# Kernel tuning notes

Measured on AMD Instinct MI355X. Metric: run time of the kernel, lower is better.

Reference implementation:

```python
import jax, jax.numpy as jnp
import numpy as np

N_NODES = 50000
N_EDGES = 800000
IN_CH = 128
OUT_CH = 64
HEADS = 4
NEG_SLOPE = 0.2


def gat_layer(x, src, dst, W, a_src, a_dst, b, n):
    """One GATConv (PyG semantics, self-loops already in src/dst).
    x:[n,Fin], W:[Fin,H*C], a_src/a_dst:[H,C], b:[H*C]. Returns [n,H*C] (concat heads)."""
    H, C = a_src.shape
    h = (x @ W).reshape(n, H, C)                      # [n,H,C]
    alpha_s = jnp.einsum('nhc,hc->nh', h, a_src)      # [n,H]
    alpha_d = jnp.einsum('nhc,hc->nh', h, a_dst)
    e = jax.nn.leaky_relu(alpha_s[src] + alpha_d[dst], NEG_SLOPE)  # [E,H]
    m = jax.ops.segment_max(e, dst, num_segments=n)   # per-dst-node max (stable softmax)
    p = jnp.exp(e - m[dst])
    denom = jax.ops.segment_sum(p, dst, num_segments=n)
    alpha = p / (denom[dst] + 1e-16)                  # [E,H]
    out = jax.ops.segment_sum(h[src] * alpha[:, :, None], dst, num_segments=n)
    return out.reshape(n, H * C) + b


def setup_inputs() -> dict:
    key = jax.random.key(0)
    ks = jax.random.split(key, 10)
    x = jax.random.normal(ks[0], (N_NODES, IN_CH), dtype=jnp.float32)
    edge_index = jax.random.randint(ks[1], (2, N_EDGES), 0, N_NODES, dtype=jnp.int64)
    s = 0.05
    W1 = jax.random.normal(ks[2], (IN_CH, HEADS * OUT_CH), dtype=jnp.float32) * s
    a_src1 = jax.random.normal(ks[3], (HEADS, OUT_CH), dtype=jnp.float32) * s
    a_dst1 = jax.random.normal(ks[4], (HEADS, OUT_CH), dtype=jnp.float32) * s
    b1 = jnp.zeros((HEADS * OUT_CH,), dtype=jnp.float32)
    W2 = jax.random.normal(ks[5], (HEADS * OUT_CH, OUT_CH), dtype=jnp.float32) * s
    a_src2 = jax.random.normal(ks[6], (1, OUT_CH), dtype=jnp.float32) * s
    a_dst2 = jax.random.normal(ks[7], (1, OUT_CH), dtype=jnp.float32) * s
    b2 = jnp.zeros((OUT_CH,), dtype=jnp.float32)
    return {"x": x, "edge_index": edge_index, "W1": W1, "a_src1": a_src1,
            "a_dst1": a_dst1, "b1": b1, "W2": W2, "a_src2": a_src2,
            "a_dst2": a_dst2, "b2": b2}


def reference(x, edge_index, W1, a_src1, a_dst1, b1, W2, a_src2, a_dst2, b2):
    n = x.shape[0]
    # PyG GATConv adds self-loops by default
    loops = jnp.arange(n, dtype=edge_index.dtype)
    src = jnp.concatenate([edge_index[0], loops])
    dst = jnp.concatenate([edge_index[1], loops])
    h = jax.nn.relu(gat_layer(x, src, dst, W1, a_src1, a_dst1, b1, n))
    return gat_layer(h, src, dst, W2, a_src2, a_dst2, b2, n)
```

## Files before the change

kernel.cpp:

```cpp
#include <hip/hip_runtime.h>
#include <math.h>

#define N_NODES   50000
#define E0_EDGES  800000
#define E_TOT     (E0_EDGES + N_NODES)
#define FIN       128
#define F1        256
#define H1        4
#define C2        64
#define NEG_SLOPE 0.2f

typedef short bf16x8 __attribute__((ext_vector_type(8)));
typedef float f32x4  __attribute__((ext_vector_type(4)));

__device__ __forceinline__ unsigned short f2bf(float f) {
  unsigned u = __float_as_uint(f);
  u = (u + 0x7FFFu + ((u >> 16) & 1u)) >> 16;
  return (unsigned short)u;
}
__device__ __forceinline__ float bf2f(unsigned short h) {
  return __uint_as_float((unsigned)h << 16);
}
__device__ __forceinline__ float leaky(float v) {
  return v >= 0.f ? v : NEG_SLOPE * v;
}

__global__ __launch_bounds__(256) void deg_kernel(
    const int* __restrict__ ei, int* __restrict__ count) {
  int e = blockIdx.x * 256 + threadIdx.x;
  if (e >= E_TOT) return;
  int dst = (e < E0_EDGES) ? ei[E0_EDGES + e] : (e - E0_EDGES);
  atomicAdd(&count[dst], 1);
}

__global__ __launch_bounds__(256) void scanA_kernel(
    const int* __restrict__ cnt, int* __restrict__ bsum, int n) {
  int i = blockIdx.x * 256 + threadIdx.x;
  int v = (i < n) ? cnt[i] : 0;
#pragma unroll
  for (int d = 1; d < 64; d <<= 1) v += __shfl_xor(v, d);
  __shared__ int ws[4];
  if ((threadIdx.x & 63) == 0) ws[threadIdx.x >> 6] = v;
  __syncthreads();
  if (threadIdx.x == 0) bsum[blockIdx.x] = ws[0] + ws[1] + ws[2] + ws[3];
}

__global__ __launch_bounds__(256) void scanB_kernel(
    const int* __restrict__ bsum, int* __restrict__ bexcl,
    int* __restrict__ off_n, int nb) {
  const int t = threadIdx.x, lane = t & 63, wid = t >> 6;
  int v = (t < nb) ? bsum[t] : 0;
  int sv = v;
#pragma unroll
  for (int d = 1; d < 64; d <<= 1) {
    int u = __shfl_up(sv, d);
    if (lane >= d) sv += u;
  }
  __shared__ int ws[4];
  if (lane == 63) ws[wid] = sv;
  __syncthreads();
  int add = 0;
  for (int k = 0; k < wid; ++k) add += ws[k];
  int incl = sv + add;
  if (t < nb) bexcl[t] = incl - v;
  if (t == 255) off_n[0] = incl;
}

__global__ __launch_bounds__(256) void scanC_kernel(
    const int* __restrict__ cnt, const int* __restrict__ bexcl,
    int* __restrict__ off, int n) {
  const int t = threadIdx.x, lane = t & 63, wid = t >> 6;
  int i = blockIdx.x * 256 + t;
  int v = (i < n) ? cnt[i] : 0;
  int sv = v;
#pragma unroll
  for (int d = 1; d < 64; d <<= 1) {
    int u = __shfl_up(sv, d);
    if (lane >= d) sv += u;
  }
  __shared__ int ws[4];
  if (lane == 63) ws[wid] = sv;
  __syncthreads();
  int add = 0;
  for (int k = 0; k < wid; ++k) add += ws[k];
  if (i < n) off[i] = sv + add - v + bexcl[blockIdx.x];
}

__global__ __launch_bounds__(256) void scatter_w_kernel(
    const int* __restrict__ ei, const int* __restrict__ offset,
    int* __restrict__ cursor, int* __restrict__ csr_src,
    const float* __restrict__ as1, const float* __restrict__ ad1,
    float* __restrict__ w4) {
  int e = blockIdx.x * 256 + threadIdx.x;
  if (e >= E_TOT) return;
  int src, dst;
  if (e < E0_EDGES) { src = ei[e]; dst = ei[E0_EDGES + e]; }
  else              { src = e - E0_EDGES; dst = src; }
  int pos = offset[dst] + atomicAdd(&cursor[dst], 1);
  csr_src[pos] = src;
  const float4 s4 = *reinterpret_cast<const float4*>(&as1[src * H1]);
  const float4 d4 = *reinterpret_cast<const float4*>(&ad1[dst * H1]);
  float4 w;
  w.x = __expf(leaky(s4.x + d4.x));
  w.y = __expf(leaky(s4.y + d4.y));
  w.z = __expf(leaky(s4.z + d4.z));
  w.w = __expf(leaky(s4.w + d4.w));
  *reinterpret_cast<float4*>(&w4[(size_t)pos * 4]) = w;
}

__global__ __launch_bounds__(256) void gemm1_kernel(
    const float* __restrict__ A, const float* __restrict__ B,
    unsigned short* __restrict__ C, float* __restrict__ as1,
    float* __restrict__ ad1, const float* __restrict__ a_s,
    const float* __restrict__ a_d, int M) {
  constexpr int K = FIN, BN = 128, KP = K + 8, NF = BN / 16;
  __shared__ unsigned short BT[BN * KP];
  const int tid = threadIdx.x, lane = tid & 63, wid = tid >> 6;
  const int gy = blockIdx.y, n0 = gy * BN;

  for (int idx = tid; idx < K * (BN / 8); idx += 256) {
    int k = idx >> 4;
    int c = idx & 15;
    const float* src = &B[(size_t)k * F1 + n0 + c * 8];
    float4 lo = *reinterpret_cast<const float4*>(src);
    float4 hi = *reinterpret_cast<const float4*>(src + 4);
    int nb = c * 8;
    BT[(nb + 0) * KP + k] = f2bf(lo.x); BT[(nb + 1) * KP + k] = f2bf(lo.y);
    BT[(nb + 2) * KP + k] = f2bf(lo.z); BT[(nb + 3) * KP + k] = f2bf(lo.w);
    BT[(nb + 4) * KP + k] = f2bf(hi.x); BT[(nb + 5) * KP + k] = f2bf(hi.y);
    BT[(nb + 6) * KP + k] = f2bf(hi.z); BT[(nb + 7) * KP + k] = f2bf(hi.w);
  }
  __syncthreads();

  const int r0 = (blockIdx.x * 4 + wid) * 16;
  if (r0 >= M) return;
  const int nlane = lane & 15;
  const int kg    = (lane >> 4) * 8;
  const int arow  = min(r0 + nlane, M - 1);

  f32x4 acc[NF];
#pragma unroll
  for (int nf = 0; nf < NF; ++nf) acc[nf] = (f32x4){0.f, 0.f, 0.f, 0.f};

  const float* ap = &A[(size_t)arow * K + kg];
#pragma unroll
  for (int kk = 0; kk < K; kk += 32) {
    float4 v0 = *reinterpret_cast<const float4*>(ap + kk);
    float4 v1 = *reinterpret_cast<const float4*>(ap + kk + 4);
    bf16x8 a;
    a[0] = (short)f2bf(v0.x); a[1] = (short)f2bf(v0.y);
    a[2] = (short)f2bf(v0.z); a[3] = (short)f2bf(v0.w);
    a[4] = (short)f2bf(v1.x); a[5] = (short)f2bf(v1.y);
    a[6] = (short)f2bf(v1.z); a[7] = (short)f2bf(v1.w);
#pragma unroll
    for (int nf = 0; nf < NF; ++nf) {
      bf16x8 b = *reinterpret_cast<const bf16x8*>(&BT[(nf * 16 + nlane) * KP + kk + kg]);
      acc[nf] = __builtin_amdgcn_mfma_f32_16x16x32_bf16(a, b, acc[nf], 0, 0, 0);
    }
  }

  const int crow = r0 + (lane >> 4) * 4;
#pragma unroll
  for (int nf = 0; nf < NF; ++nf) {
    const int cc = n0 + nf * 16 + nlane;
#pragma unroll
    for (int j = 0; j < 4; ++j) {
      int rr = crow + j;
      if (rr < M) C[(size_t)rr * F1 + cc] = f2bf(acc[nf][j]);
    }
  }

#pragma unroll
  for (int j = 0; j < 4; ++j) {
    float ps0 = 0.f, ps1 = 0.f, pd0 = 0.f, pd1 = 0.f;
#pragma unroll
    for (int nf = 0; nf < NF; ++nf) {
      int col = n0 + nf * 16 + nlane;
      float v = acc[nf][j];
      float sc = a_s[col], dc = a_d[col];
      if (nf < 4) { ps0 = fmaf(v, sc, ps0); pd0 = fmaf(v, dc, pd0); }
      else        { ps1 = fmaf(v, sc, ps1); pd1 = fmaf(v, dc, pd1); }
    }
#pragma unroll
    for (int d = 1; d < 16; d <<= 1) {
      ps0 += __shfl_xor(ps0, d); ps1 += __shfl_xor(ps1, d);
      pd0 += __shfl_xor(pd0, d); pd1 += __shfl_xor(pd1, d);
    }
    int row = crow + j;
    if (nlane == 0 && row < M) {
      float2 s2 = {ps0, ps1}, d2 = {pd0, pd1};
      *reinterpret_cast<float2*>(&as1[row * 4 + gy * 2]) = s2;
      *reinterpret_cast<float2*>(&ad1[row * 4 + gy * 2]) = d2;
    }
  }
}

__global__ __launch_bounds__(256) void gemm2_kernel(
    const unsigned short* __restrict__ A, const float* __restrict__ B,
    unsigned short* __restrict__ C, float* __restrict__ as2,
    float* __restrict__ ad2, const float* __restrict__ a_s,
    const float* __restrict__ a_d, int M) {
  constexpr int K = F1, BN = 64, KP = K + 8, NF = BN / 16;
  __shared__ unsigned short BT[BN * KP];
  const int tid = threadIdx.x, lane = tid & 63, wid = tid >> 6;

  for (int idx = tid; idx < K * (BN / 8); idx += 256) {
    int k = idx >> 3;
    int c = idx & 7;
    const float* src = &B[(size_t)k * C2 + c * 8];
    float4 lo = *reinterpret_cast<const float4*>(src);
    float4 hi = *reinterpret_cast<const float4*>(src + 4);
    int nb = c * 8;
    BT[(nb + 0) * KP + k] = f2bf(lo.x); BT[(nb + 1) * KP + k] = f2bf(lo.y);
    BT[(nb + 2) * KP + k] = f2bf(lo.z); BT[(nb + 3) * KP + k] = f2bf(lo.w);
    BT[(nb + 4) * KP + k] = f2bf(hi.x); BT[(nb + 5) * KP + k] = f2bf(hi.y);
    BT[(nb + 6) * KP + k] = f2bf(hi.z); BT[(nb + 7) * KP + k] = f2bf(hi.w);
  }
  __syncthreads();

  const int r0 = (blockIdx.x * 4 + wid) * 16;
  if (r0 >= M) return;
  const int nlane = lane & 15;
  const int kg    = (lane >> 4) * 8;
  const int arow  = min(r0 + nlane, M - 1);

  f32x4 acc[NF];
#pragma unroll
  for (int nf = 0; nf < NF; ++nf) acc[nf] = (f32x4){0.f, 0.f, 0.f, 0.f};

  const unsigned short* ap = &A[(size_t)arow * K + kg];
#pragma unroll
  for (int kk = 0; kk < K; kk += 32) {
    bf16x8 a = *reinterpret_cast<const bf16x8*>(ap + kk);
#pragma unroll
    for (int nf = 0; nf < NF; ++nf) {
      bf16x8 b = *reinterpret_cast<const bf16x8*>(&BT[(nf * 16 + nlane) * KP + kk + kg]);
      acc[nf] = __builtin_amdgcn_mfma_f32_16x16x32_bf16(a, b, acc[nf], 0, 0, 0);
    }
  }

  const int crow = r0 + (lane >> 4) * 4;
#pragma unroll
  for (int nf = 0; nf < NF; ++nf) {
    const int cc = nf * 16 + nlane;
#pragma unroll
    for (int j = 0; j < 4; ++j) {
      int rr = crow + j;
      if (rr < M) C[(size_t)rr * C2 + cc] = f2bf(acc[nf][j]);
    }
  }

#pragma unroll
  for (int j = 0; j < 4; ++j) {
    float ps = 0.f, pd = 0.f;
#pragma unroll
    for (int nf = 0; nf < NF; ++nf) {
      int col = nf * 16 + nlane;
      float v = acc[nf][j];
      ps = fmaf(v, a_s[col], ps);
      pd = fmaf(v, a_d[col], pd);
    }
#pragma unroll
    for (int d = 1; d < 16; d <<= 1) {
      ps += __shfl_xor(ps, d);
      pd += __shfl_xor(pd, d);
    }
    int row = crow + j;
    if (nlane == 0 && row < M) { as2[row] = ps; ad2[row] = pd; }
  }
}

__global__ __launch_bounds__(256) void aggregate1_kernel(
    const unsigned short* __restrict__ h1b, const float* __restrict__ w4,
    const int* __restrict__ csr_src, const int* __restrict__ offset,
    const float* __restrict__ b1, unsigned short* __restrict__ out1b,
    int node0, int n) {
  const int lane = threadIdx.x & 63;
  const int node = node0 + blockIdx.x * 4 + (threadIdx.x >> 6);
  if (node >= n) return;
  const int beg = offset[node], end = offset[node + 1];
  const int hl = lane >> 4;
  const unsigned loff = (unsigned)(lane * 4);

  float4 acc = make_float4(0.f, 0.f, 0.f, 0.f);
  float den = 0.f;
  int e = beg;
  for (; e + 7 < end; e += 8) {
    int s[8];
    float wv[8];
    ushort4 r[8];
#pragma unroll
    for (int i = 0; i < 8; ++i) s[i] = csr_src[e + i];
#pragma unroll
    for (int i = 0; i < 8; ++i) wv[i] = w4[(size_t)(e + i) * 4 + hl];
#pragma unroll
    for (int i = 0; i < 8; ++i)
      r[i] = *reinterpret_cast<const ushort4*>(h1b + (unsigned)(s[i] * F1) + loff);
#pragma unroll
    for (int i = 0; i < 8; ++i) {
      den += wv[i];
      acc.x = fmaf(wv[i], bf2f(r[i].x), acc.x);
      acc.y = fmaf(wv[i], bf2f(r[i].y), acc.y);
      acc.z = fmaf(wv[i], bf2f(r[i].z), acc.z);
      acc.w = fmaf(wv[i], bf2f(r[i].w), acc.w);
    }
  }
  for (; e < end; ++e) {
    const int s0 = csr_src[e];
    const float w = w4[(size_t)e * 4 + hl];
    den += w;
    const ushort4 r0 = *reinterpret_cast<const ushort4*>(h1b + (unsigned)(s0 * F1) + loff);
    acc.x = fmaf(w, bf2f(r0.x), acc.x);
    acc.y = fmaf(w, bf2f(r0.y), acc.y);
    acc.z = fmaf(w, bf2f(r0.z), acc.z);
    acc.w = fmaf(w, bf2f(r0.w), acc.w);
  }
  const float inv = 1.f / (den + 1e-16f);
  const float4 bb = *reinterpret_cast<const float4*>(&b1[lane * 4]);
  ushort4 ob;
  ob.x = f2bf(fmaxf(fmaf(acc.x, inv, bb.x), 0.f));
  ob.y = f2bf(fmaxf(fmaf(acc.y, inv, bb.y), 0.f));
  ob.z = f2bf(fmaxf(fmaf(acc.z, inv, bb.z), 0.f));
  ob.w = f2bf(fmaxf(fmaf(acc.w, inv, bb.w), 0.f));
  *reinterpret_cast<ushort4*>(&out1b[(size_t)node * F1 + lane * 4]) = ob;
}

__global__ __launch_bounds__(256) void aggregate2_kernel(
    const unsigned short* __restrict__ h2b, const float* __restrict__ as,
    const float* __restrict__ ad, const int* __restrict__ csr_src,
    const int* __restrict__ offset, const float* __restrict__ b2,
    float* __restrict__ out, int n) {
  const int lane = threadIdx.x & 63;
  const int node = blockIdx.x * 4 + (threadIdx.x >> 6);
  if (node >= n) return;
  const int beg = offset[node], end = offset[node + 1];
  const float adv = ad[node];

  float acc = 0.f;
  float den = 0.f;
  int e = beg;
  for (; e + 7 < end; e += 8) {
    int s[8];
    unsigned short r[8];
    float a[8];
#pragma unroll
    for (int i = 0; i < 8; ++i) s[i] = csr_src[e + i];
#pragma unroll
    for (int i = 0; i < 8; ++i) r[i] = h2b[(unsigned)(s[i] * C2) + lane];
#pragma unroll
    for (int i = 0; i < 8; ++i) a[i] = as[s[i]];
#pragma unroll
    for (int i = 0; i < 8; ++i) {
      const float w = __expf(leaky(a[i] + adv));
      den += w;
      acc = fmaf(w, bf2f(r[i]), acc);
    }
  }
  for (; e < end; ++e) {
    const int s0 = csr_src[e];
    const float w = __expf(leaky(as[s0] + adv));
    den += w;
    acc = fmaf(w, bf2f(h2b[(unsigned)(s0 * C2) + lane]), acc);
  }
  out[(size_t)node * C2 + lane] = fmaf(acc, 1.f / (den + 1e-16f), b2[lane]);
}

extern "C" void kernel_launch(void* const* d_in, const int* in_sizes, int n_in,
                              void* d_out, int out_size, void* d_ws, size_t ws_size,
                              hipStream_t stream) {
  const float* x      = (const float*)d_in[0];
  const int*   ei     = (const int*)d_in[1];
  const float* W1     = (const float*)d_in[2];
  const float* a_src1 = (const float*)d_in[3];
  const float* a_dst1 = (const float*)d_in[4];
  const float* b1     = (const float*)d_in[5];
  const float* W2     = (const float*)d_in[6];
  const float* a_src2 = (const float*)d_in[7];
  const float* a_dst2 = (const float*)d_in[8];
  const float* b2     = (const float*)d_in[9];
  float*       out    = (float*)d_out;

  const int n = N_NODES;
  const int nchunks = (n + 255) / 256;

  char* w = (char*)d_ws;
  unsigned short* h1b   = (unsigned short*)w; w += (size_t)n * F1 * 2;
  unsigned short* out1b = (unsigned short*)w; w += (size_t)n * F1 * 2;
  float*          w4    = (float*)w;          w += (size_t)E_TOT * 4 * 4;
  float*          as1   = (float*)w;          w += (size_t)n * H1 * 4;
  float*          ad1   = (float*)w;          w += (size_t)n * H1 * 4;
  float*          as2   = (float*)w;          w += 200192;
  float*          ad2   = (float*)w;          w += 200192;
  int*            cnt   = (int*)w;            w += 200192;
  int*            cur   = (int*)w;            w += 200192;
  int*            off   = (int*)w;            w += 200704;
  int*            bsum  = (int*)w;            w += 1024;
  int*            bexcl = (int*)w;            w += 1024;
  int*            csr   = (int*)w;            w += 3400192;
  unsigned short* h2b   = h1b;

  hipMemsetAsync(cnt, 0, 2 * 200192, stream);
  deg_kernel<<<(E_TOT + 255) / 256, 256, 0, stream>>>(ei, cnt);
  scanA_kernel<<<nchunks, 256, 0, stream>>>(cnt, bsum, n);
  scanB_kernel<<<1, 256, 0, stream>>>(bsum, bexcl, &off[n], nchunks);
  scanC_kernel<<<nchunks, 256, 0, stream>>>(cnt, bexcl, off, n);

  {
    dim3 grid((n + 63) / 64, 2);
    gemm1_kernel<<<grid, 256, 0, stream>>>(x, W1, h1b, as1, ad1, a_src1, a_dst1, n);
  }

  scatter_w_kernel<<<(E_TOT + 255) / 256, 256, 0, stream>>>(
      ei, off, cur, csr, as1, ad1, w4);

  {
    const int half = 25000;
    aggregate1_kernel<<<(half + 3) / 4, 256, 0, stream>>>(
        h1b, w4, csr, off, b1, out1b, 0, half);
    aggregate1_kernel<<<(n - half + 3) / 4, 256, 0, stream>>>(
        h1b, w4, csr, off, b1, out1b, half, n);
  }

  {
    dim3 grid((n + 63) / 64, 1);
    gemm2_kernel<<<grid, 256, 0, stream>>>(out1b, W2, h2b, as2, ad2, a_src2, a_dst2, n);
  }
  aggregate2_kernel<<<(n + 3) / 4, 256, 0, stream>>>(h2b, as2, ad2, csr, off, b2, out, n);
}
```

Measured before the change: 333.6 us.

## Split edge-weight computation into CSR-ordered kernels for both layers

The scatter kernel now only builds the CSR source array, and the layer-1 attention weights move to a separate per-node kernel that walks CSR order. Writes to w4 become contiguous instead of scattered by atomic position, and scatter can run before gemm1. Layer 2 gets a similar precompute kernel for its edge weights, so aggregate2 reads w2 sequentially instead of gathering as2 and computing exp inline. This adds two launches and an extra pass over csr_src.

```diff
diff --git a/kernel.cpp b/kernel.cpp
--- a/kernel.cpp
+++ b/kernel.cpp
@@ -86,11 +86,9 @@
   if (i < n) off[i] = sv + add - v + bexcl[blockIdx.x];
 }
 
-__global__ __launch_bounds__(256) void scatter_w_kernel(
+__global__ __launch_bounds__(256) void scatter_kernel(
     const int* __restrict__ ei, const int* __restrict__ offset,
-    int* __restrict__ cursor, int* __restrict__ csr_src,
-    const float* __restrict__ as1, const float* __restrict__ ad1,
-    float* __restrict__ w4) {
+    int* __restrict__ cursor, int* __restrict__ csr_src) {
   int e = blockIdx.x * 256 + threadIdx.x;
   if (e >= E_TOT) return;
   int src, dst;
@@ -98,14 +96,40 @@
   else              { src = e - E0_EDGES; dst = src; }
   int pos = offset[dst] + atomicAdd(&cursor[dst], 1);
   csr_src[pos] = src;
-  const float4 s4 = *reinterpret_cast<const float4*>(&as1[src * H1]);
-  const float4 d4 = *reinterpret_cast<const float4*>(&ad1[dst * H1]);
-  float4 w;
-  w.x = __expf(leaky(s4.x + d4.x));
-  w.y = __expf(leaky(s4.y + d4.y));
-  w.z = __expf(leaky(s4.z + d4.z));
-  w.w = __expf(leaky(s4.w + d4.w));
-  *reinterpret_cast<float4*>(&w4[(size_t)pos * 4]) = w;
+}
+
+__global__ __launch_bounds__(256) void w1_kernel(
+    const float* __restrict__ as1, const float* __restrict__ ad1,
+    const int* __restrict__ csr_src, const int* __restrict__ offset,
+    float* __restrict__ w4, int n) {
+  const int lane = threadIdx.x & 63;
+  const int node = blockIdx.x * 4 + (threadIdx.x >> 6);
+  if (node >= n) return;
+  const int beg = offset[node], end = offset[node + 1];
+  const float4 d4 = *reinterpret_cast<const float4*>(&ad1[node * H1]);
+  for (int e = beg + lane; e < end; e += 64) {
+    const int s = csr_src[e];
+    const float4 s4 = *reinterpret_cast<const float4*>(&as1[s * H1]);
+    float4 w;
+    w.x = __expf(leaky(s4.x + d4.x));
+    w.y = __expf(leaky(s4.y + d4.y));
+    w.z = __expf(leaky(s4.z + d4.z));
+    w.w = __expf(leaky(s4.w + d4.w));
+    *reinterpret_cast<float4*>(&w4[(size_t)e * 4]) = w;
+  }
+}
+
+__global__ __launch_bounds__(256) void w2_kernel(
+    const float* __restrict__ as2, const float* __restrict__ ad2,
+    const int* __restrict__ csr_src, const int* __restrict__ offset,
+    float* __restrict__ w2, int n) {
+  const int lane = threadIdx.x & 63;
+  const int node = blockIdx.x * 4 + (threadIdx.x >> 6);
+  if (node >= n) return;
+  const int beg = offset[node], end = offset[node + 1];
+  const float dv = ad2[node];
+  for (int e = beg + lane; e < end; e += 64)
+    w2[e] = __expf(leaky(as2[csr_src[e]] + dv));
 }
 
 __global__ __launch_bounds__(256) void gemm1_kernel(
@@ -326,39 +350,36 @@
 }
 
 __global__ __launch_bounds__(256) void aggregate2_kernel(
-    const unsigned short* __restrict__ h2b, const float* __restrict__ as,
-    const float* __restrict__ ad, const int* __restrict__ csr_src,
-    const int* __restrict__ offset, const float* __restrict__ b2,
-    float* __restrict__ out, int n) {
+    const unsigned short* __restrict__ h2b, const float* __restrict__ w2,
+    const int* __restrict__ csr_src, const int* __restrict__ offset,
+    const float* __restrict__ b2, float* __restrict__ out, int n) {
   const int lane = threadIdx.x & 63;
   const int node = blockIdx.x * 4 + (threadIdx.x >> 6);
   if (node >= n) return;
   const int beg = offset[node], end = offset[node + 1];
-  const float adv = ad[node];
 
   float acc = 0.f;
   float den = 0.f;
   int e = beg;
   for (; e + 7 < end; e += 8) {
     int s[8];
+    float wv[8];
     unsigned short r[8];
-    float a[8];
 #pragma unroll
     for (int i = 0; i < 8; ++i) s[i] = csr_src[e + i];
 #pragma unroll
+    for (int i = 0; i < 8; ++i) wv[i] = w2[e + i];
+#pragma unroll
     for (int i = 0; i < 8; ++i) r[i] = h2b[(unsigned)(s[i] * C2) + lane];
 #pragma unroll
-    for (int i = 0; i < 8; ++i) a[i] = as[s[i]];
-#pragma unroll
     for (int i = 0; i < 8; ++i) {
-      const float w = __expf(leaky(a[i] + adv));
-      den += w;
-      acc = fmaf(w, bf2f(r[i]), acc);
+      den += wv[i];
+      acc = fmaf(wv[i], bf2f(r[i]), acc);
     }
   }
   for (; e < end; ++e) {
     const int s0 = csr_src[e];
-    const float w = __expf(leaky(as[s0] + adv));
+    const float w = w2[e];
     den += w;
     acc = fmaf(w, bf2f(h2b[(unsigned)(s0 * C2) + lane]), acc);
   }
@@ -398,21 +419,20 @@
   int*            bexcl = (int*)w;            w += 1024;
   int*            csr   = (int*)w;            w += 3400192;
   unsigned short* h2b   = h1b;
+  float*          w2    = w4;
 
   hipMemsetAsync(cnt, 0, 2 * 200192, stream);
   deg_kernel<<<(E_TOT + 255) / 256, 256, 0, stream>>>(ei, cnt);
   scanA_kernel<<<nchunks, 256, 0, stream>>>(cnt, bsum, n);
   scanB_kernel<<<1, 256, 0, stream>>>(bsum, bexcl, &off[n], nchunks);
   scanC_kernel<<<nchunks, 256, 0, stream>>>(cnt, bexcl, off, n);
+  scatter_kernel<<<(E_TOT + 255) / 256, 256, 0, stream>>>(ei, off, cur, csr);
 
   {
     dim3 grid((n + 63) / 64, 2);
     gemm1_kernel<<<grid, 256, 0, stream>>>(x, W1, h1b, as1, ad1, a_src1, a_dst1, n);
   }
-
-  scatter_w_kernel<<<(E_TOT + 255) / 256, 256, 0, stream>>>(
-      ei, off, cur, csr, as1, ad1, w4);
-
+  w1_kernel<<<(n + 3) / 4, 256, 0, stream>>>(as1, ad1, csr, off, w4, n);
   {
     const int half = 25000;
     aggregate1_kernel<<<(half + 3) / 4, 256, 0, stream>>>(
@@ -425,5 +445,6 @@
     dim3 grid((n + 63) / 64, 1);
     gemm2_kernel<<<grid, 256, 0, stream>>>(out1b, W2, h2b, as2, ad2, a_src2, a_dst2, n);
   }
-  aggregate2_kernel<<<(n + 3) / 4, 256, 0, stream>>>(h2b, as2, ad2, csr, off, b2, out, n);
-}
+  w2_kernel<<<(n + 3) / 4, 256, 0, stream>>>(as2, ad2, csr, off, w2, n);
+  aggregate2_kernel<<<(n + 3) / 4, 256, 0, stream>>>(h2b, w2, csr, off, b2, out, n);
+}
```

Result: slower. 354.0 us (+6.1%).

## Record edge ranks in degree pass and fuse CSR scatter into GEMM1 launch

Applied to the files above, without the earlier changes.

The degree-count kernel now stores each edge's atomic rank, so the CSR scatter needs no second atomic cursor. That scatter runs as extra blocks inside the GEMM1 launch so the two overlap. Edge weights are computed in a separate node-centric kernel over CSR order, which reads the destination score once per node, and aggregate1 runs as a single launch instead of two halves. In exchange there is an extra rank buffer write and read, and one more pass over the CSR edges.

```diff
diff --git a/kernel.cpp b/kernel.cpp
--- a/kernel.cpp
+++ b/kernel.cpp
@@ -10,6 +10,10 @@
 #define C2        64
 #define NEG_SLOPE 0.2f
 
+#define NBX1      ((N_NODES + 63) / 64)
+#define GEMM1_BLOCKS (NBX1 * 2)
+#define SCAT_BLOCKS  ((E_TOT + 255) / 256)
+
 typedef short bf16x8 __attribute__((ext_vector_type(8)));
 typedef float f32x4  __attribute__((ext_vector_type(4)));
 
@@ -26,11 +30,12 @@
 }
 
 __global__ __launch_bounds__(256) void deg_kernel(
-    const int* __restrict__ ei, int* __restrict__ count) {
+    const int* __restrict__ ei, int* __restrict__ count,
+    int* __restrict__ rank) {
   int e = blockIdx.x * 256 + threadIdx.x;
   if (e >= E_TOT) return;
   int dst = (e < E0_EDGES) ? ei[E0_EDGES + e] : (e - E0_EDGES);
-  atomicAdd(&count[dst], 1);
+  rank[e] = atomicAdd(&count[dst], 1);
 }
 
 __global__ __launch_bounds__(256) void scanA_kernel(
@@ -86,37 +91,31 @@
   if (i < n) off[i] = sv + add - v + bexcl[blockIdx.x];
 }
 
-__global__ __launch_bounds__(256) void scatter_w_kernel(
-    const int* __restrict__ ei, const int* __restrict__ offset,
-    int* __restrict__ cursor, int* __restrict__ csr_src,
-    const float* __restrict__ as1, const float* __restrict__ ad1,
-    float* __restrict__ w4) {
-  int e = blockIdx.x * 256 + threadIdx.x;
-  if (e >= E_TOT) return;
-  int src, dst;
-  if (e < E0_EDGES) { src = ei[e]; dst = ei[E0_EDGES + e]; }
-  else              { src = e - E0_EDGES; dst = src; }
-  int pos = offset[dst] + atomicAdd(&cursor[dst], 1);
-  csr_src[pos] = src;
-  const float4 s4 = *reinterpret_cast<const float4*>(&as1[src * H1]);
-  const float4 d4 = *reinterpret_cast<const float4*>(&ad1[dst * H1]);
-  float4 w;
-  w.x = __expf(leaky(s4.x + d4.x));
-  w.y = __expf(leaky(s4.y + d4.y));
-  w.z = __expf(leaky(s4.z + d4.z));
-  w.w = __expf(leaky(s4.w + d4.w));
-  *reinterpret_cast<float4*>(&w4[(size_t)pos * 4]) = w;
-}
-
-__global__ __launch_bounds__(256) void gemm1_kernel(
+__global__ __launch_bounds__(256) void gemm1_scatter_kernel(
     const float* __restrict__ A, const float* __restrict__ B,
     unsigned short* __restrict__ C, float* __restrict__ as1,
     float* __restrict__ ad1, const float* __restrict__ a_s,
-    const float* __restrict__ a_d, int M) {
+    const float* __restrict__ a_d, int M,
+    const int* __restrict__ ei, const int* __restrict__ offset,
+    const int* __restrict__ rank, int* __restrict__ csr_src) {
   constexpr int K = FIN, BN = 128, KP = K + 8, NF = BN / 16;
   __shared__ unsigned short BT[BN * KP];
+  const int bid = blockIdx.x;
+
+  if (bid >= GEMM1_BLOCKS) {
+    int e = (bid - GEMM1_BLOCKS) * 256 + threadIdx.x;
+    if (e >= E_TOT) return;
+    int src, dst;
+    if (e < E0_EDGES) { src = ei[e]; dst = ei[E0_EDGES + e]; }
+    else              { src = e - E0_EDGES; dst = src; }
+    csr_src[offset[dst] + rank[e]] = src;
+    return;
+  }
+
+  const int bx = bid % NBX1;
+  const int gy = bid / NBX1;
   const int tid = threadIdx.x, lane = tid & 63, wid = tid >> 6;
-  const int gy = blockIdx.y, n0 = gy * BN;
+  const int n0 = gy * BN;
 
   for (int idx = tid; idx < K * (BN / 8); idx += 256) {
     int k = idx >> 4;
@@ -132,7 +131,7 @@
   }
   __syncthreads();
 
-  const int r0 = (blockIdx.x * 4 + wid) * 16;
+  const int r0 = (bx * 4 + wid) * 16;
   if (r0 >= M) return;
   const int nlane = lane & 15;
   const int kg    = (lane >> 4) * 8;
@@ -192,6 +191,27 @@
       *reinterpret_cast<float2*>(&as1[row * 4 + gy * 2]) = s2;
       *reinterpret_cast<float2*>(&ad1[row * 4 + gy * 2]) = d2;
     }
+  }
+}
+
+__global__ __launch_bounds__(256) void w1_kernel(
+    const float* __restrict__ as1, const float* __restrict__ ad1,
+    const int* __restrict__ csr_src, const int* __restrict__ offset,
+    float* __restrict__ w4, int n) {
+  const int lane = threadIdx.x & 63;
+  const int node = blockIdx.x * 4 + (threadIdx.x >> 6);
+  if (node >= n) return;
+  const int beg = offset[node], end = offset[node + 1];
+  const float4 d4 = *reinterpret_cast<const float4*>(&ad1[node * H1]);
+  for (int e = beg + lane; e < end; e += 64) {
+    const int s = csr_src[e];
+    const float4 s4 = *reinterpret_cast<const float4*>(&as1[s * H1]);
+    float4 w;
+    w.x = __expf(leaky(s4.x + d4.x));
+    w.y = __expf(leaky(s4.y + d4.y));
+    w.z = __expf(leaky(s4.z + d4.z));
+    w.w = __expf(leaky(s4.w + d4.w));
+    *reinterpret_cast<float4*>(&w4[(size_t)e * 4]) = w;
   }
 }
 
@@ -273,10 +293,9 @@
 __global__ __launch_bounds__(256) void aggregate1_kernel(
     const unsigned short* __restrict__ h1b, const float* __restrict__ w4,
     const int* __restrict__ csr_src, const int* __restrict__ offset,
-    const float* __restrict__ b1, unsigned short* __restrict__ out1b,
-    int node0, int n) {
+    const float* __restrict__ b1, unsigned short* __restrict__ out1b, int n) {
   const int lane = threadIdx.x & 63;
-  const int node = node0 + blockIdx.x * 4 + (threadIdx.x >> 6);
+  const int node = blockIdx.x * 4 + (threadIdx.x >> 6);
   if (node >= n) return;
   const int beg = offset[node], end = offset[node + 1];
   const int hl = lane >> 4;
@@ -392,38 +411,26 @@
   float*          as2   = (float*)w;          w += 200192;
   float*          ad2   = (float*)w;          w += 200192;
   int*            cnt   = (int*)w;            w += 200192;
-  int*            cur   = (int*)w;            w += 200192;
   int*            off   = (int*)w;            w += 200704;
   int*            bsum  = (int*)w;            w += 1024;
   int*            bexcl = (int*)w;            w += 1024;
+  int*            rank  = (int*)w;            w += 3400192;
   int*            csr   = (int*)w;            w += 3400192;
   unsigned short* h2b   = h1b;
 
-  hipMemsetAsync(cnt, 0, 2 * 200192, stream);
-  deg_kernel<<<(E_TOT + 255) / 256, 256, 0, stream>>>(ei, cnt);
+  hipMemsetAsync(cnt, 0, 200192, stream);
+  deg_kernel<<<SCAT_BLOCKS, 256, 0, stream>>>(ei, cnt, rank);
   scanA_kernel<<<nchunks, 256, 0, stream>>>(cnt, bsum, n);
   scanB_kernel<<<1, 256, 0, stream>>>(bsum, bexcl, &off[n], nchunks);
   scanC_kernel<<<nchunks, 256, 0, stream>>>(cnt, bexcl, off, n);
 
-  {
-    dim3 grid((n + 63) / 64, 2);
-    gemm1_kernel<<<grid, 256, 0, stream>>>(x, W1, h1b, as1, ad1, a_src1, a_dst1, n);
-  }
-
-  scatter_w_kernel<<<(E_TOT + 255) / 256, 256, 0, stream>>>(
-      ei, off, cur, csr, as1, ad1, w4);
-
-  {
-    const int half = 25000;
-    aggregate1_kernel<<<(half + 3) / 4, 256, 0, stream>>>(
-        h1b, w4, csr, off, b1, out1b, 0, half);
-    aggregate1_kernel<<<(n - half + 3) / 4, 256, 0, stream>>>(
-        h1b, w4, csr, off, b1, out1b, half, n);
-  }
-
-  {
-    dim3 grid((n + 63) / 64, 1);
-    gemm2_kernel<<<grid, 256, 0, stream>>>(out1b, W2, h2b, as2, ad2, a_src2, a_dst2, n);
-  }
+  gemm1_scatter_kernel<<<GEMM1_BLOCKS + SCAT_BLOCKS, 256, 0, stream>>>(
+      x, W1, h1b, as1, ad1, a_src1, a_dst1, n, ei, off, rank, csr);
+
+  w1_kernel<<<(n + 3) / 4, 256, 0, stream>>>(as1, ad1, csr, off, w4, n);
+  aggregate1_kernel<<<(n + 3) / 4, 256, 0, stream>>>(h1b, w4, csr, off, b1, out1b, n);
+
+  gemm2_kernel<<<(n + 63) / 64, 256, 0, stream>>>(out1b, W2, h2b, as2, ad2,
+                                                  a_src2, a_dst2, n);
   aggregate2_kernel<<<(n + 3) / 4, 256, 0, stream>>>(h2b, as2, ad2, csr, off, b2, out, n);
 }
```

New measurement: 297.2 us. -10.9%, faster.
